# Performance work log

Measured on AMD Instinct MI355X. Metric: run time of the kernel, lower is better.

Reference implementation:

```python
import jax, jax.numpy as jnp
import numpy as np

TAU = 2.0        # LIF membrane time constant
VTH = 1.0        # firing threshold
ALPHA = 4.0      # surrogate sigmoid sharpness
BN_EPS = 1e-5

@jax.custom_vjp
def heaviside_surrogate(x):
    # Forward: hard threshold. Backward: sigmoid surrogate gradient (alpha=4).
    return (x >= 0.0).astype(x.dtype)

def _hs_fwd(x):
    return heaviside_surrogate(x), x

def _hs_bwd(x, g):
    s = jax.nn.sigmoid(ALPHA * x)
    return (g * ALPHA * s * (1.0 - s),)

heaviside_surrogate.defvjp(_hs_fwd, _hs_bwd)


def setup_inputs() -> dict:
    key = jax.random.key(0)
    k1, k2 = jax.random.split(key)
    B, Cin, T, Cout = 64, 512, 1024, 256
    x = jax.random.normal(k1, (B, Cin, T), dtype=jnp.float32)
    W = jax.random.normal(k2, (Cout, Cin), dtype=jnp.float32) * (1.0 / np.sqrt(Cin))
    gamma = jnp.ones((Cout,), dtype=jnp.float32)
    beta = jnp.zeros((Cout,), dtype=jnp.float32)
    run_mean = jnp.zeros((Cout,), dtype=jnp.float32)
    run_var = jnp.ones((Cout,), dtype=jnp.float32)
    return {"x": x, "W": W, "gamma": gamma, "beta": beta,
            "run_mean": run_mean, "run_var": run_var}


def reference(x, W, gamma, beta, run_mean, run_var):
    # Dropout is identity in eval mode.
    # conv1d, kernel_size=1, no bias -> pointwise GEMM over channels: [B,Cin,T] -> [B,Cout,T]
    y = jnp.einsum('bct,oc->bot', x, W)
    # BatchNorm1d (inference, running stats), per-channel affine
    inv = jax.lax.rsqrt(run_var + BN_EPS)
    y = (y - run_mean[None, :, None]) * (inv * gamma)[None, :, None] + beta[None, :, None]
    # LIF recurrence over the time dim (last axis), hard reset to 0, detach_reset.
    yt = jnp.transpose(y, (2, 0, 1))  # [T, B, Cout]

    def step(v, x_t):
        v = v + (x_t - v) / TAU              # decay_input charge
        s = heaviside_surrogate(v - VTH)     # spike via surrogate threshold
        v = v * (1.0 - jax.lax.stop_gradient(s))  # hard reset (detached)
        return v, s

    v0 = jnp.zeros(yt.shape[1:], dtype=yt.dtype)
    _, spikes = jax.lax.scan(step, v0, yt)   # spikes: [T, B, Cout]
    # out.mean(dim=-1) == spike rate over time
    return spikes.mean(axis=0)               # [B, Cout]
```

## Files before the change

kernel.cpp:

```cpp
#include <hip/hip_runtime.h>
#include <math.h>

typedef _Float16 f16;
typedef __attribute__((ext_vector_type(8)))  _Float16 f16v8;
typedef __attribute__((ext_vector_type(4)))  __fp16   h16v4;
typedef __attribute__((ext_vector_type(16))) float    f32x16;
typedef __attribute__((ext_vector_type(4)))  float    f32x4;

namespace {
constexpr int kB = 64, kCin = 512, kT = 1024, kCout = 256;
constexpr size_t kYBytes     = (size_t)kB * kT * kCout * 4;
constexpr size_t kWfragBytes = (size_t)32 * 8 * 2 * 64 * 16;
constexpr size_t kSBytes     = kCout * 4;
constexpr size_t kWsNeed     = kYBytes + kWfragBytes + kSBytes;
}

__global__ void wsplit16_kernel(const float* __restrict__ W, const float* __restrict__ gamma,
                                const float* __restrict__ rvar,
                                f16* __restrict__ wfrag, float* __restrict__ sarr) {
    const int kc = blockIdx.x, osub = blockIdx.y, p = blockIdx.z;
    const int lane = threadIdx.x;
    const int o  = osub * 32 + (lane & 31);
    const int kb = kc * 16 + (lane >> 5) * 8;
    f16v8 frag;
#pragma unroll
    for (int j = 0; j < 8; ++j) {
        const float w = 32.0f * W[o * kCin + kb + j];
        const f16 h = (f16)w;
        const float r = w - (float)h;
        const f16 l = (f16)(r * 2048.0f);
        frag[j] = p ? l : h;
    }
    *reinterpret_cast<f16v8*>(wfrag + ((size_t)((kc * 8 + osub) * 2 + p) * 64 + lane) * 8) = frag;
    if (kc == 0 && osub == 0 && p == 0) {
#pragma unroll
        for (int j = 0; j < 4; ++j) {
            const int oo = j * 64 + lane;
            sarr[oo] = (float)((double)gamma[oo] / sqrt((double)rvar[oo] + 1e-5));
        }
    }
}

__global__ __launch_bounds__(256, 2)
void gemm_f16_kernel(const float* __restrict__ x, const f16* __restrict__ wfrag,
                     const float* __restrict__ sarr, const float* __restrict__ rmean,
                     const float* __restrict__ beta, float* __restrict__ yt) {
    __shared__ unsigned int Bd[4][64 * 20];

    const int tid  = threadIdx.x;
    const int lane = tid & 63;
    const int wave = tid >> 6;
    const int n = lane & 31, q = lane >> 5;
    const int b   = blockIdx.y;
    const int tg0 = blockIdx.x * 64;
    const float* __restrict__ xb = x + ((size_t)b << 19);
    const f16v8* __restrict__ wf = reinterpret_cast<const f16v8*>(wfrag);

    const int st_t = tid & 63;
    const int kpp  = wave;
    const int st_sw = (st_t >> 3) & 3;
    const int wr_base = 20 * st_t + 2 * (kpp & 1);
    const int s0 = ((0 + (kpp >> 1)) ^ st_sw) * 4;
    const int s1 = ((2 + (kpp >> 1)) ^ st_sw) * 4;

    f32x16 accA[2][2] = {};
    f32x16 accB[2][2] = {};
    f16v8  af[2][2][2];
    float  xq[4][4];

    auto loadX = [&](int kc, float (&xd)[4]) {
        const float* px = xb + (size_t)(kc * 16 + 4 * kpp) * kT + tg0 + st_t;
#pragma unroll
        for (int r = 0; r < 4; ++r) xd[r] = px[(size_t)r * kT];
    };
    auto loadA = [&](int kc, f16v8 (&ad)[2][2]) {
#pragma unroll
        for (int i = 0; i < 2; ++i)
#pragma unroll
            for (int p = 0; p < 2; ++p)
                ad[i][p] = wf[(size_t)((kc * 8 + wave * 2 + i) * 2 + p) * 64 + lane];
    };
    auto stage = [&](int buf, const float (&xd)[4]) {
        auto h01 = __builtin_amdgcn_cvt_pkrtz(xd[0], xd[1]);
        auto h23 = __builtin_amdgcn_cvt_pkrtz(xd[2], xd[3]);
        auto l01 = __builtin_amdgcn_cvt_pkrtz((xd[0] - (float)h01[0]) * 2048.0f,
                                              (xd[1] - (float)h01[1]) * 2048.0f);
        auto l23 = __builtin_amdgcn_cvt_pkrtz((xd[2] - (float)h23[0]) * 2048.0f,
                                              (xd[3] - (float)h23[1]) * 2048.0f);
        h16v4 hv, lv;
        hv[0] = h01[0]; hv[1] = h01[1]; hv[2] = h23[0]; hv[3] = h23[1];
        lv[0] = l01[0]; lv[1] = l01[1]; lv[2] = l23[0]; lv[3] = l23[1];
        *reinterpret_cast<h16v4*>(&Bd[buf][wr_base + s0]) = hv;
        *reinterpret_cast<h16v4*>(&Bd[buf][wr_base + s1]) = lv;
    };
    auto domfma = [&](int buf, const f16v8 (&ad)[2][2]) {
        __builtin_amdgcn_s_setprio(1);
#pragma unroll
        for (int s = 0; s < 2; ++s) {
            const int t = s * 32 + n;
            const int sw = (t >> 3) & 3;
            const f16v8 bh = *reinterpret_cast<const f16v8*>(&Bd[buf][20 * t + 4 * ((0 + q) ^ sw)]);
            const f16v8 bl = *reinterpret_cast<const f16v8*>(&Bd[buf][20 * t + 4 * ((2 + q) ^ sw)]);
#pragma unroll
            for (int i = 0; i < 2; ++i) {
                accA[i][s] = __builtin_amdgcn_mfma_f32_32x32x16_f16(ad[i][0], bh, accA[i][s], 0, 0, 0);
                accB[i][s] = __builtin_amdgcn_mfma_f32_32x32x16_f16(ad[i][0], bl, accB[i][s], 0, 0, 0);
                accB[i][s] = __builtin_amdgcn_mfma_f32_32x32x16_f16(ad[i][1], bh, accB[i][s], 0, 0, 0);
            }
        }
        __builtin_amdgcn_s_setprio(0);
    };

    loadX(0, xq[0]); loadX(1, xq[1]); loadX(2, xq[2]); loadX(3, xq[3]);
    loadA(0, af[0]);
    stage(0, xq[0]);
    stage(1, xq[1]);
    asm volatile("s_waitcnt lgkmcnt(0)\n\ts_barrier" ::: "memory");

    for (int kc4 = 0; kc4 < 8; ++kc4) {
#pragma unroll
        for (int u = 0; u < 4; ++u) {
            const int kc = kc4 * 4 + u;
            if (kc < 31) loadA(kc + 1, af[(u + 1) & 1]);
            if (kc < 30) stage((u + 2) & 3, xq[(u + 2) & 3]);
            if (kc < 28) loadX(kc + 4, xq[u]);
            domfma(u, af[u & 1]);
            if (u & 1)
                asm volatile("s_waitcnt lgkmcnt(0)\n\ts_barrier" ::: "memory");
        }
    }

#pragma unroll
    for (int i = 0; i < 2; ++i) {
        f32x4 sv[4], mv[4], bv[4];
#pragma unroll
        for (int g = 0; g < 4; ++g) {
            const int og = wave * 64 + i * 32 + g * 8 + q * 4;
            sv[g] = *reinterpret_cast<const f32x4*>(sarr + og);
            mv[g] = *reinterpret_cast<const f32x4*>(rmean + og);
            bv[g] = *reinterpret_cast<const f32x4*>(beta + og);
        }
#pragma unroll
        for (int s = 0; s < 2; ++s) {
            const f32x16 v = accA[i][s] + accB[i][s] * 4.8828125e-4f;
            const size_t t = (size_t)tg0 + s * 32 + n;
#pragma unroll
            for (int g = 0; g < 4; ++g)
#pragma unroll
                for (int r2 = 0; r2 < 4; ++r2) {
                    const int o = wave * 64 + i * 32 + g * 8 + q * 4 + r2;
                    const float val = (v[4 * g + r2] * 0.03125f - mv[g][r2]) * sv[g][r2] + bv[g][r2];
                    yt[(((size_t)b << 8) + (size_t)o) * 1024 + t] = val;
                }
        }
    }
}

__global__ __launch_bounds__(64)
void lif_kernel(const float* __restrict__ yt, float* __restrict__ out) {
    const int b = blockIdx.x >> 2;
    const int o = ((blockIdx.x & 3) << 6) + threadIdx.x;
    const f32x4* __restrict__ row =
        reinterpret_cast<const f32x4*>(yt) + (((size_t)b << 8) + (size_t)o) * 256;
    float v = 0.f;
    int cnt = 0;
    f32x4 qb[16];
#pragma unroll
    for (int u = 0; u < 16; ++u) qb[u] = row[u];
    for (int jj = 0; jj < 15; ++jj) {
#pragma unroll
        for (int u = 0; u < 16; ++u) {
            const f32x4 cv = qb[u];
            qb[u] = row[jj * 16 + u + 16];
#pragma unroll
            for (int e = 0; e < 4; ++e) {
                v = v + (cv[e] - v) * 0.5f;
                if (v - 1.0f >= 0.0f) { ++cnt; v = 0.f; }
            }
        }
    }
#pragma unroll
    for (int u = 0; u < 16; ++u) {
        const f32x4 cv = qb[u];
#pragma unroll
        for (int e = 0; e < 4; ++e) {
            v = v + (cv[e] - v) * 0.5f;
            if (v - 1.0f >= 0.0f) { ++cnt; v = 0.f; }
        }
    }
    out[((size_t)b << 8) + o] = (float)cnt * (1.0f / 1024.0f);
}

namespace fb {
constexpr int kOTile = 32, kTTile = 128, kCc = 64;
constexpr int kNtt = kT / kTTile, kNcc = kCin / kCc, kYPad = 132;
}

__global__ void wt_transpose_kernel(const float* __restrict__ W, float* __restrict__ Wt) {
    int idx = blockIdx.x * 256 + threadIdx.x;
    int c = idx >> 8, o = idx & 255;
    Wt[idx] = W[o * kCin + c];
}

__global__ __launch_bounds__(256, 2)
void snn_fused_kernel(const float* __restrict__ x, const float* __restrict__ Wt,
                      const float* __restrict__ gamma, const float* __restrict__ beta,
                      const float* __restrict__ rmean, const float* __restrict__ rvar,
                      float* __restrict__ out) {
    using namespace fb;
    __shared__ float xs[kCc][kTTile];
    __shared__ float ws[kCc][kOTile];
    __shared__ float ytile[kOTile][kYPad];
    __shared__ float sarr[kOTile], barr[kOTile], marr[kOTile], vstate[kOTile];
    __shared__ int scnt[kOTile];
    const int tid = threadIdx.x, tx = tid & 31, ty = tid >> 5;
    const int b = blockIdx.y, o_blk = blockIdx.x * kOTile;
    if (tid < kOTile) {
        const int o = o_blk + tid;
        const double dinv = 1.0 / sqrt((double)rvar[o] + 1e-5);
        sarr[tid] = (float)(dinv * (double)gamma[o]);
        barr[tid] = beta[o]; marr[tid] = rmean[o];
        vstate[tid] = 0.0f; scnt[tid] = 0;
    }
    __syncthreads();
    const float* xb = x + (size_t)b * kCin * kT;
    for (int tt = 0; tt < kNtt; ++tt) {
        float acc[4][4];
#pragma unroll
        for (int i = 0; i < 4; ++i)
#pragma unroll
            for (int j = 0; j < 4; ++j) acc[i][j] = 0.0f;
        const int t0 = tt * kTTile;
        for (int cc = 0; cc < kNcc; ++cc) {
#pragma unroll
            for (int k = 0; k < 8; ++k) {
                const int f = tid + 256 * k;
                const int c = f >> 5, tq = f & 31;
                *reinterpret_cast<float4*>(&xs[c][tq * 4]) = *reinterpret_cast<const float4*>(
                    xb + (size_t)(cc * kCc + c) * kT + t0 + tq * 4);
            }
#pragma unroll
            for (int k = 0; k < 2; ++k) {
                const int f = tid + 256 * k;
                const int c = f >> 3, oq = f & 7;
                *reinterpret_cast<float4*>(&ws[c][oq * 4]) = *reinterpret_cast<const float4*>(
                    Wt + (size_t)(cc * kCc + c) * kCout + o_blk + oq * 4);
            }
            __syncthreads();
#pragma unroll 8
            for (int c = 0; c < kCc; ++c) {
                const float4 xv = *reinterpret_cast<const float4*>(&xs[c][tx * 4]);
                const float4 wv = *reinterpret_cast<const float4*>(&ws[c][ty * 4]);
                const float xf[4] = {xv.x, xv.y, xv.z, xv.w};
                const float wf4[4] = {wv.x, wv.y, wv.z, wv.w};
#pragma unroll
                for (int i = 0; i < 4; ++i)
#pragma unroll
                    for (int j = 0; j < 4; ++j) acc[i][j] += wf4[i] * xf[j];
            }
            __syncthreads();
        }
#pragma unroll
        for (int i = 0; i < 4; ++i) {
            const int o = ty * 4 + i;
            const float s = sarr[o], bb2 = barr[o], m = marr[o];
#pragma unroll
            for (int j = 0; j < 4; ++j) ytile[o][tx * 4 + j] = (acc[i][j] - m) * s + bb2;
        }
        __syncthreads();
        if (tid < kOTile) {
            float vv = vstate[tid];
            int cnt = 0;
#pragma unroll 4
            for (int t = 0; t < kTTile; ++t) {
                const float yv = ytile[tid][t];
                vv = vv + (yv - vv) * 0.5f;
                if (vv - 1.0f >= 0.0f) { cnt++; vv = 0.0f; }
            }
            vstate[tid] = vv; scnt[tid] += cnt;
        }
        __syncthreads();
    }
    if (tid < kOTile) out[b * kCout + o_blk + tid] = (float)scnt[tid] * (1.0f / 1024.0f);
}

extern "C" void kernel_launch(void* const* d_in, const int* in_sizes, int n_in,
                              void* d_out, int out_size, void* d_ws, size_t ws_size,
                              hipStream_t stream) {
    const float* x     = (const float*)d_in[0];
    const float* W     = (const float*)d_in[1];
    const float* gamma = (const float*)d_in[2];
    const float* beta  = (const float*)d_in[3];
    const float* rmean = (const float*)d_in[4];
    const float* rvar  = (const float*)d_in[5];
    float* out = (float*)d_out;

    if (ws_size >= kWsNeed) {
        float* yt    = (float*)d_ws;
        f16*   wfrag = (f16*)((char*)d_ws + kYBytes);
        float* sarr  = (float*)((char*)d_ws + kYBytes + kWfragBytes);
        wsplit16_kernel<<<dim3(32, 8, 2), 64, 0, stream>>>(W, gamma, rvar, wfrag, sarr);
        gemm_f16_kernel<<<dim3(16, 64), 256, 0, stream>>>(x, wfrag, sarr, rmean, beta, yt);
        lif_kernel<<<256, 64, 0, stream>>>(yt, out);
    } else {
        float* Wt = (float*)d_ws;
        wt_transpose_kernel<<<(kCin * kCout) / 256, 256, 0, stream>>>(W, Wt);
        snn_fused_kernel<<<dim3(kCout / fb::kOTile, kB), 256, 0, stream>>>(
            x, Wt, gamma, beta, rmean, rvar, out);
    }
}
```

Before: 255.9 us.

## Split output channels across two blocks to halve accumulators and raise occupancy

Each GEMM block now covers 128 output channels instead of 256, with a grid z-dimension of 2. Every wave holds one 32-channel tile, which halves the accumulator and A-fragment registers and lets launch bounds ask for 4 blocks per CU instead of 2. The aim is more latency hiding through occupancy. The cost is that each x tile is loaded from global memory and converted to f16 twice, doubling that traffic and the conversion work.

```diff
diff --git a/kernel.cpp b/kernel.cpp
--- a/kernel.cpp
+++ b/kernel.cpp
@@ -41,7 +41,7 @@
     }
 }
 
-__global__ __launch_bounds__(256, 2)
+__global__ __launch_bounds__(256, 4)
 void gemm_f16_kernel(const float* __restrict__ x, const f16* __restrict__ wfrag,
                      const float* __restrict__ sarr, const float* __restrict__ rmean,
                      const float* __restrict__ beta, float* __restrict__ yt) {
@@ -53,6 +53,7 @@
     const int n = lane & 31, q = lane >> 5;
     const int b   = blockIdx.y;
     const int tg0 = blockIdx.x * 64;
+    const int osg = blockIdx.z * 4 + wave;
     const float* __restrict__ xb = x + ((size_t)b << 19);
     const f16v8* __restrict__ wf = reinterpret_cast<const f16v8*>(wfrag);
 
@@ -63,9 +64,9 @@
     const int s0 = ((0 + (kpp >> 1)) ^ st_sw) * 4;
     const int s1 = ((2 + (kpp >> 1)) ^ st_sw) * 4;
 
-    f32x16 accA[2][2] = {};
-    f32x16 accB[2][2] = {};
-    f16v8  af[2][2][2];
+    f32x16 accA[2] = {};
+    f32x16 accB[2] = {};
+    f16v8  af[2][2];
     float  xq[4][4];
 
     auto loadX = [&](int kc, float (&xd)[4]) {
@@ -73,12 +74,10 @@
 #pragma unroll
         for (int r = 0; r < 4; ++r) xd[r] = px[(size_t)r * kT];
     };
-    auto loadA = [&](int kc, f16v8 (&ad)[2][2]) {
-#pragma unroll
-        for (int i = 0; i < 2; ++i)
-#pragma unroll
-            for (int p = 0; p < 2; ++p)
-                ad[i][p] = wf[(size_t)((kc * 8 + wave * 2 + i) * 2 + p) * 64 + lane];
+    auto loadA = [&](int kc, f16v8 (&ad)[2]) {
+#pragma unroll
+        for (int p = 0; p < 2; ++p)
+            ad[p] = wf[(size_t)((kc * 8 + osg) * 2 + p) * 64 + lane];
     };
     auto stage = [&](int buf, const float (&xd)[4]) {
         auto h01 = __builtin_amdgcn_cvt_pkrtz(xd[0], xd[1]);
@@ -93,7 +92,7 @@
         *reinterpret_cast<h16v4*>(&Bd[buf][wr_base + s0]) = hv;
         *reinterpret_cast<h16v4*>(&Bd[buf][wr_base + s1]) = lv;
     };
-    auto domfma = [&](int buf, const f16v8 (&ad)[2][2]) {
+    auto domfma = [&](int buf, const f16v8 (&ad)[2]) {
         __builtin_amdgcn_s_setprio(1);
 #pragma unroll
         for (int s = 0; s < 2; ++s) {
@@ -101,12 +100,9 @@
             const int sw = (t >> 3) & 3;
             const f16v8 bh = *reinterpret_cast<const f16v8*>(&Bd[buf][20 * t + 4 * ((0 + q) ^ sw)]);
             const f16v8 bl = *reinterpret_cast<const f16v8*>(&Bd[buf][20 * t + 4 * ((2 + q) ^ sw)]);
-#pragma unroll
-            for (int i = 0; i < 2; ++i) {
-                accA[i][s] = __builtin_amdgcn_mfma_f32_32x32x16_f16(ad[i][0], bh, accA[i][s], 0, 0, 0);
-                accB[i][s] = __builtin_amdgcn_mfma_f32_32x32x16_f16(ad[i][0], bl, accB[i][s], 0, 0, 0);
-                accB[i][s] = __builtin_amdgcn_mfma_f32_32x32x16_f16(ad[i][1], bh, accB[i][s], 0, 0, 0);
-            }
+            accA[s] = __builtin_amdgcn_mfma_f32_32x32x16_f16(ad[0], bh, accA[s], 0, 0, 0);
+            accB[s] = __builtin_amdgcn_mfma_f32_32x32x16_f16(ad[0], bl, accB[s], 0, 0, 0);
+            accB[s] = __builtin_amdgcn_mfma_f32_32x32x16_f16(ad[1], bh, accB[s], 0, 0, 0);
         }
         __builtin_amdgcn_s_setprio(0);
     };
@@ -131,27 +127,21 @@
     }
 
 #pragma unroll
-    for (int i = 0; i < 2; ++i) {
-        f32x4 sv[4], mv[4], bv[4];
+    for (int s = 0; s < 2; ++s) {
+        const f32x16 v = accA[s] + accB[s] * 4.8828125e-4f;
+        const size_t t = (size_t)tg0 + s * 32 + n;
 #pragma unroll
         for (int g = 0; g < 4; ++g) {
-            const int og = wave * 64 + i * 32 + g * 8 + q * 4;
-            sv[g] = *reinterpret_cast<const f32x4*>(sarr + og);
-            mv[g] = *reinterpret_cast<const f32x4*>(rmean + og);
-            bv[g] = *reinterpret_cast<const f32x4*>(beta + og);
-        }
-#pragma unroll
-        for (int s = 0; s < 2; ++s) {
-            const f32x16 v = accA[i][s] + accB[i][s] * 4.8828125e-4f;
-            const size_t t = (size_t)tg0 + s * 32 + n;
-#pragma unroll
-            for (int g = 0; g < 4; ++g)
-#pragma unroll
-                for (int r2 = 0; r2 < 4; ++r2) {
-                    const int o = wave * 64 + i * 32 + g * 8 + q * 4 + r2;
-                    const float val = (v[4 * g + r2] * 0.03125f - mv[g][r2]) * sv[g][r2] + bv[g][r2];
-                    yt[(((size_t)b << 8) + (size_t)o) * 1024 + t] = val;
-                }
+            const int og = osg * 32 + g * 8 + q * 4;
+            const f32x4 sv = *reinterpret_cast<const f32x4*>(sarr + og);
+            const f32x4 mv = *reinterpret_cast<const f32x4*>(rmean + og);
+            const f32x4 bv = *reinterpret_cast<const f32x4*>(beta + og);
+#pragma unroll
+            for (int r2 = 0; r2 < 4; ++r2) {
+                const int o = og + r2;
+                const float val = (v[4 * g + r2] * 0.03125f - mv[r2]) * sv[r2] + bv[r2];
+                yt[(((size_t)b << 8) + (size_t)o) * 1024 + t] = val;
+            }
         }
     }
 }
@@ -300,7 +290,7 @@
         f16*   wfrag = (f16*)((char*)d_ws + kYBytes);
         float* sarr  = (float*)((char*)d_ws + kYBytes + kWfragBytes);
         wsplit16_kernel<<<dim3(32, 8, 2), 64, 0, stream>>>(W, gamma, rvar, wfrag, sarr);
-        gemm_f16_kernel<<<dim3(16, 64), 256, 0, stream>>>(x, wfrag, sarr, rmean, beta, yt);
+        gemm_f16_kernel<<<dim3(16, 64, 2), 256, 0, stream>>>(x, wfrag, sarr, rmean, beta, yt);
         lif_kernel<<<256, 64, 0, stream>>>(yt, out);
     } else {
         float* Wt = (float*)d_ws;
```

Result: slower. 269.1 us (+5.2%).
